# Kernel tuning notes

Hardware: AMD Instinct MI355X
Metric: run time of the kernel (lower is better)

Reference implementation:

```python
import jax, jax.numpy as jnp
import numpy as np

D_MODEL, N_HEADS, N_LEVELS, N_POINTS, ROI = 256, 8, 4, 4, 7
SHAPES = np.array([[100, 150], [50, 75], [25, 38], [13, 19]], dtype=np.int32)
STARTS = np.array([0, 15000, 18750, 19700], dtype=np.int32)


def setup_inputs() -> dict:
    key = jax.random.key(0)
    ks = jax.random.split(key, 12)
    N, Lq = 4, 300
    Len_in = int((SHAPES[:, 0] * SHAPES[:, 1]).sum())  # 19947
    C = D_MODEL
    roi_dim = ROI * ROI * C  # 12544
    np_dim = N_HEADS * N_LEVELS * N_POINTS
    inp = {
        'query': jax.random.normal(ks[0], (N, Lq, C), jnp.float32),
        'reference_points': jax.random.uniform(ks[1], (N, Lq, N_LEVELS, 4), jnp.float32, 0.05, 0.95),
        'input_flatten': jax.random.normal(ks[2], (N, Len_in, C), jnp.float32),
        'input_spatial_shapes': jnp.asarray(SHAPES),
        'input_level_start_index': jnp.asarray(STARTS),
        'input_padding_mask': jnp.zeros((N, Len_in), jnp.bool_),
        'Wv': jax.random.normal(ks[3], (C, C), jnp.float32) / np.sqrt(C),
        'bv': jnp.zeros((C,), jnp.float32),
        'Wp': jax.random.normal(ks[4], (roi_dim, np_dim * 2), jnp.float32) / np.sqrt(roi_dim),
        'bp': jnp.zeros((np_dim * 2,), jnp.float32),
        'Ww': jax.random.normal(ks[5], (roi_dim, np_dim), jnp.float32) / np.sqrt(roi_dim),
        'bw': jnp.zeros((np_dim,), jnp.float32),
        'Wo': jax.random.normal(ks[6], (C, C), jnp.float32) / np.sqrt(C),
        'bo': jnp.zeros((C,), jnp.float32),
    }
    return inp


def _bilinear(img, y, x):
    # img: (H, W, C); y, x: arbitrary shape. Zero padding outside, matches
    # grid_sample(align_corners=False, padding_mode='zeros') / roi_align bilinear.
    H, W = img.shape[0], img.shape[1]
    y0 = jnp.floor(y)
    x0 = jnp.floor(x)
    wy1 = y - y0
    wx1 = x - x0

    def corner(yi, xi, w):
        valid = (yi >= 0) & (yi <= H - 1) & (xi >= 0) & (xi <= W - 1)
        yc = jnp.clip(yi, 0, H - 1).astype(jnp.int32)
        xc = jnp.clip(xi, 0, W - 1).astype(jnp.int32)
        return img[yc, xc] * (w * valid)[..., None]

    return (corner(y0, x0, (1 - wy1) * (1 - wx1))
            + corner(y0, x0 + 1, (1 - wy1) * wx1)
            + corner(y0 + 1, x0, wy1 * (1 - wx1))
            + corner(y0 + 1, x0 + 1, wy1 * wx1))


def _forward(query, reference_points, input_flatten, shapes, starts, padding_mask,
             Wv, bv, Wp, bp, Ww, bw, Wo, bo):
    N, Len_in, C = input_flatten.shape
    Lq = query.shape[1]
    Dh = C // N_HEADS

    # value projection + padding mask
    value = input_flatten @ Wv + bv
    value = jnp.where(padding_mask[..., None], 0.0, value)

    # --- ROI align on level-0 feature map (output 7x7, aligned=True, sampling_ratio=1) ---
    H0, W0 = int(shapes[0, 0]), int(shapes[0, 1])
    v0 = value[:, :H0 * W0].reshape(N, H0, W0, C)
    cx, cy, w, h = [reference_points[:, :, 0, i] for i in range(4)]
    x1 = (cx - 0.5 * w) * W0 - 0.5  # aligned=True offset
    y1 = (cy - 0.5 * h) * H0 - 0.5
    bin_w = (w * W0) / ROI
    bin_h = (h * H0) / ROI
    ctr = jnp.arange(ROI, dtype=jnp.float32) + 0.5  # bin centers
    sx = x1[..., None] + bin_w[..., None] * ctr  # (N, Lq, 7)
    sy = y1[..., None] + bin_h[..., None] * ctr
    yg = jnp.broadcast_to(sy[:, :, :, None], (N, Lq, ROI, ROI))
    xg = jnp.broadcast_to(sx[:, :, None, :], (N, Lq, ROI, ROI))
    roi = jax.vmap(_bilinear)(v0, yg, xg)  # (N, Lq, 7, 7, C)
    roi_flat = roi.reshape(N, Lq, ROI * ROI * C)

    # --- learned sampling points + softmax weights (key_points_sampling_module) ---
    pr = jnp.tanh(roi_flat @ Wp + bp).reshape(N, Lq, N_HEADS, N_LEVELS, N_POINTS, 2)
    logits = (roi_flat @ Ww + bw).reshape(N, Lq, N_HEADS, N_LEVELS * N_POINTS)
    attn = jax.nn.softmax(logits, axis=-1).reshape(N, Lq, N_HEADS, N_LEVELS, N_POINTS)

    # points = ref_center + offsets * ref_wh * 0.5, normalized [0,1], (x, y)
    ref = reference_points  # (N, Lq, L, 4)
    pts = ref[:, :, None, :, None, :2] + pr * ref[:, :, None, :, None, 2:] * 0.5

    # --- multi-scale deformable bilinear sampling ---
    out = jnp.zeros((N, Lq, N_HEADS, Dh), value.dtype)
    value_h = value.reshape(N, Len_in, N_HEADS, Dh)
    for l in range(N_LEVELS):
        Hl, Wl = int(shapes[l, 0]), int(shapes[l, 1])
        s = int(starts[l])
        vl = value_h[:, s:s + Hl * Wl].reshape(N, Hl, Wl, N_HEADS, Dh)
        vl = vl.transpose(0, 3, 1, 2, 4)  # (N, H, Hl, Wl, Dh)
        px = pts[:, :, :, l, :, 0] * Wl - 0.5  # grid_sample align_corners=False
        py = pts[:, :, :, l, :, 1] * Hl - 0.5
        px = px.transpose(0, 2, 1, 3)  # (N, H, Lq, P)
        py = py.transpose(0, 2, 1, 3)
        samp = jax.vmap(jax.vmap(_bilinear))(vl, py, px)  # (N, H, Lq, P, Dh)
        wl = attn[:, :, :, l, :].transpose(0, 2, 1, 3)  # (N, H, Lq, P)
        out = out + jnp.einsum('nhqpd,nhqp->nqhd', samp, wl)

    out = out.reshape(N, Lq, C)
    return out @ Wo + bo


def reference(query, reference_points, input_flatten, input_spatial_shapes,
              input_level_start_index, input_padding_mask,
              Wv, bv, Wp, bp, Ww, bw, Wo, bo):
    shapes = np.asarray(input_spatial_shapes)
    starts = np.asarray(input_level_start_index)
    return _forward(query, reference_points, input_flatten, shapes, starts,
                    input_padding_mask, Wv, bv, Wp, bp, Ww, bw, Wo, bo)
```

## Files before the change

kernel.cpp:

```cpp
#include <hip/hip_runtime.h>
#include <hip/hip_bf16.h>
#include <math.h>

#define NB 4
#define LQ 300
#define CDIM 256
#define NH 8
#define DH 32
#define NL 4
#define NP 4
#define ROI_ 7
#define LEN_IN 19947
#define H0 100
#define W0 150
#define ROI_DIM (ROI_*ROI_*CDIM)
#define NQ_TOT (NB*LQ)
#define QPB 3

#define MPAD2 1280
#define NDIM 384
#define KCH_TOT 196
#define MT_N 10
#define NT_N 3

#define VTOT (NB*LEN_IN)
#define VMT  624

__device__ __constant__ int d_HL[4] = {100, 50, 25, 13};
__device__ __constant__ int d_WL[4] = {150, 75, 38, 19};
__device__ __constant__ int d_ST[4] = {0, 15000, 18750, 19700};

typedef __attribute__((ext_vector_type(8))) short short8;
typedef __attribute__((ext_vector_type(4))) float f32x4;

__device__ __forceinline__ unsigned short f2bf(float f) {
    unsigned int u = __float_as_uint(f);
    unsigned int r = (u + 0x7fffu + ((u >> 16) & 1u)) >> 16;
    return (unsigned short)r;
}
__device__ __forceinline__ float bf2f(unsigned short s) {
    return __uint_as_float(((unsigned int)s) << 16);
}

__device__ __forceinline__ void mfma_32x64(
    const unsigned short* aH, const unsigned short* aL,
    const unsigned short* bH, const unsigned short* bL,
    int wm, int wn, int lr, int kb, f32x4 acc[2][4])
{
    #pragma unroll
    for (int kk = 0; kk < 2; ++kk) {
        short8 ah[2], al[2];
        #pragma unroll
        for (int i = 0; i < 2; ++i) {
            int row = wm * 32 + i * 16 + lr;
            int off = (row * 128 + kk * 64 + kb * 16) ^ ((row & 7) << 4);
            ah[i] = *(const short8*)((const char*)aH + off);
            al[i] = *(const short8*)((const char*)aL + off);
        }
        #pragma unroll
        for (int j = 0; j < 4; ++j) {
            int col = wn * 64 + j * 16 + lr;
            int off = (col * 128 + kk * 64 + kb * 16) ^ ((col & 7) << 4);
            short8 bh = *(const short8*)((const char*)bH + off);
            short8 bl = *(const short8*)((const char*)bL + off);
            #pragma unroll
            for (int i = 0; i < 2; ++i) {
                acc[i][j] = __builtin_amdgcn_mfma_f32_16x16x32_bf16(ah[i], bh, acc[i][j], 0, 0, 0);
                acc[i][j] = __builtin_amdgcn_mfma_f32_16x16x32_bf16(ah[i], bl, acc[i][j], 0, 0, 0);
                acc[i][j] = __builtin_amdgcn_mfma_f32_16x16x32_bf16(al[i], bh, acc[i][j], 0, 0, 0);
            }
        }
    }
}

__global__ __launch_bounds__(256) void k_wvsplit(
    const float* __restrict__ Wv,
    unsigned short* __restrict__ WvTh,
    unsigned short* __restrict__ WvTl)
{
    __shared__ float tile[32][33];
    int k0 = blockIdx.x * 32, c0 = blockIdx.y * 32;
    int tx = threadIdx.x & 31, ty = threadIdx.x >> 5;
    #pragma unroll
    for (int i = 0; i < 4; ++i)
        tile[ty + i * 8][tx] = Wv[(size_t)(k0 + ty + i * 8) * CDIM + c0 + tx];
    __syncthreads();
    #pragma unroll
    for (int i = 0; i < 4; ++i) {
        int c = c0 + ty + i * 8, k = k0 + tx;
        float v = tile[tx][ty + i * 8];
        unsigned short hb = f2bf(v);
        WvTh[(size_t)c * CDIM + k] = hb;
        WvTl[(size_t)c * CDIM + k] = f2bf(v - bf2f(hb));
    }
}

__global__ __launch_bounds__(512, 4) void k_value_mfma(
    const float* __restrict__ inp,
    const unsigned char* __restrict__ mask,
    const unsigned short* __restrict__ WvTh,
    const unsigned short* __restrict__ WvTl,
    const float* __restrict__ bv,
    float* __restrict__ value)
{
    __shared__ unsigned short aH[128 * 64], aL[128 * 64];
    __shared__ unsigned short bH[128 * 64], bL[128 * 64];
    const int row0 = blockIdx.y * 128;
    const int n0 = blockIdx.x * 128;
    const int tid = threadIdx.x;
    const int lane = tid & 63;
    const int wid = tid >> 6;
    const int wm = wid >> 1, wn = wid & 1;
    const int lr = lane & 15, kb = lane >> 4;

    f32x4 acc[2][4];
    #pragma unroll
    for (int i = 0; i < 2; ++i)
        #pragma unroll
        for (int j = 0; j < 4; ++j) acc[i][j] = f32x4{0.f, 0.f, 0.f, 0.f};

    int rc[2], ko[2], growA[2];
    #pragma unroll
    for (int i2 = 0; i2 < 2; ++i2) {
        int slot = tid + i2 * 512;
        rc[i2] = slot >> 3; ko[i2] = slot & 7;
        int g = row0 + rc[i2];
        growA[i2] = (g < VTOT) ? g : (VTOT - 1);
    }

    float4 fa0[2], fa1[2];
    short8 pbh[2], pbl[2];
    #pragma unroll
    for (int i2 = 0; i2 < 2; ++i2) {
        const float* src = inp + (size_t)growA[i2] * CDIM + ko[i2] * 8;
        fa0[i2] = *(const float4*)src;
        fa1[i2] = *(const float4*)(src + 4);
        size_t gb = (size_t)(n0 + rc[i2]) * CDIM + ko[i2] * 8;
        pbh[i2] = *(const short8*)(WvTh + gb);
        pbl[i2] = *(const short8*)(WvTl + gb);
    }

    #pragma unroll
    for (int ch = 0; ch < 4; ++ch) {
        __syncthreads();
        #pragma unroll
        for (int i2 = 0; i2 < 2; ++i2) {
            float f[8] = {fa0[i2].x, fa0[i2].y, fa0[i2].z, fa0[i2].w,
                          fa1[i2].x, fa1[i2].y, fa1[i2].z, fa1[i2].w};
            short8 h, l;
            #pragma unroll
            for (int e = 0; e < 8; ++e) {
                unsigned short hb = f2bf(f[e]);
                h[e] = (short)hb;
                l[e] = (short)f2bf(f[e] - bf2f(hb));
            }
            int off = (rc[i2] * 128 + ko[i2] * 16) ^ ((rc[i2] & 7) << 4);
            *(short8*)((char*)aH + off) = h;
            *(short8*)((char*)aL + off) = l;
            *(short8*)((char*)bH + off) = pbh[i2];
            *(short8*)((char*)bL + off) = pbl[i2];
        }
        __syncthreads();
        if (ch < 3) {
            const int k0n = (ch + 1) * 64;
            #pragma unroll
            for (int i2 = 0; i2 < 2; ++i2) {
                const float* src = inp + (size_t)growA[i2] * CDIM + k0n + ko[i2] * 8;
                fa0[i2] = *(const float4*)src;
                fa1[i2] = *(const float4*)(src + 4);
                size_t gb = (size_t)(n0 + rc[i2]) * CDIM + k0n + ko[i2] * 8;
                pbh[i2] = *(const short8*)(WvTh + gb);
                pbl[i2] = *(const short8*)(WvTl + gb);
            }
        }
        mfma_32x64(aH, aL, bH, bL, wm, wn, lr, kb, acc);
    }

    #pragma unroll
    for (int j = 0; j < 4; ++j) {
        int c = n0 + wn * 64 + j * 16 + lr;
        float b = bv[c];
        #pragma unroll
        for (int i = 0; i < 2; ++i) {
            int q = row0 + wm * 32 + i * 16 + kb * 4;
            #pragma unroll
            for (int e = 0; e < 4; ++e) {
                int row = q + e;
                if (row < VTOT) {
                    float v = acc[i][j][e] + b;
                    if (mask[row]) v = 0.f;
                    value[(size_t)row * CDIM + c] = v;
                }
            }
        }
    }
}

__global__ __launch_bounds__(256) void k_value_proj(
    const float* __restrict__ inp,
    const unsigned char* __restrict__ mask,
    const float* __restrict__ Wv,
    const float* __restrict__ bv,
    float* __restrict__ value)
{
    const int ROWS = 16;
    __shared__ float a_s[ROWS][CDIM];
    const int total = VTOT;
    int row0 = blockIdx.x * ROWS;
    int tid = threadIdx.x;

    #pragma unroll
    for (int r = 0; r < ROWS; ++r) {
        int row = row0 + r;
        a_s[r][tid] = (row < total) ? inp[(size_t)row * CDIM + tid] : 0.f;
    }
    __syncthreads();

    float acc[ROWS];
    #pragma unroll
    for (int r = 0; r < ROWS; ++r) acc[r] = 0.f;

    for (int k = 0; k < CDIM; k += 4) {
        float w0 = Wv[(k + 0) * CDIM + tid];
        float w1 = Wv[(k + 1) * CDIM + tid];
        float w2 = Wv[(k + 2) * CDIM + tid];
        float w3 = Wv[(k + 3) * CDIM + tid];
        #pragma unroll
        for (int r = 0; r < ROWS; ++r) {
            float4 av = *(const float4*)&a_s[r][k];
            acc[r] = fmaf(av.x, w0, fmaf(av.y, w1, fmaf(av.z, w2, fmaf(av.w, w3, acc[r]))));
        }
    }

    float b = bv[tid];
    #pragma unroll
    for (int r = 0; r < ROWS; ++r) {
        int row = row0 + r;
        if (row < total) {
            float v = acc[r] + b;
            if (mask[row]) v = 0.f;
            value[(size_t)row * CDIM + tid] = v;
        }
    }
}

__global__ __launch_bounds__(256) void k_roi_split(
    const float* __restrict__ value,
    const float* __restrict__ refp,
    unsigned short* __restrict__ roiH,
    unsigned short* __restrict__ roiL)
{
    int q = blockIdx.x;
    int t = threadIdx.x;
    int g = t & 31;
    int p8 = t >> 5;

    if (q >= NQ_TOT) {
        short8 z = {0, 0, 0, 0, 0, 0, 0, 0};
        for (int i = p8; i < 49; i += 8) {
            *(short8*)(roiH + (size_t)q * ROI_DIM + i * 256 + g * 8) = z;
            *(short8*)(roiL + (size_t)q * ROI_DIM + i * 256 + g * 8) = z;
        }
        return;
    }
    int n = q / LQ;
    const float* rp = refp + (size_t)q * NL * 4;
    float cx = rp[0], cy = rp[1], w = rp[2], h = rp[3];
    float x1 = (cx - 0.5f * w) * W0 - 0.5f;
    float y1 = (cy - 0.5f * h) * H0 - 0.5f;
    float binw = w * W0 / ROI_;
    float binh = h * H0 / ROI_;
    const float* v0 = value + (size_t)n * LEN_IN * CDIM;

    for (int i = p8; i < 49; i += 8) {
        int r = i / ROI_, c = i % ROI_;
        float sy = y1 + binh * (r + 0.5f);
        float sx = x1 + binw * (c + 0.5f);
        float y0f = floorf(sy), x0f = floorf(sx);
        float wy1 = sy - y0f, wx1 = sx - x0f;
        int y0 = (int)y0f, x0 = (int)x0f;

        float acc[8];
        #pragma unroll
        for (int e = 0; e < 8; ++e) acc[e] = 0.f;

        #pragma unroll
        for (int dy = 0; dy <= 1; ++dy) {
            #pragma unroll
            for (int dx = 0; dx <= 1; ++dx) {
                int yy = y0 + dy, xx = x0 + dx;
                if (yy >= 0 && yy < H0 && xx >= 0 && xx < W0) {
                    float wgt = (dy ? wy1 : 1.f - wy1) * (dx ? wx1 : 1.f - wx1);
                    const float* src = v0 + ((size_t)(yy * W0 + xx)) * CDIM + g * 8;
                    float4 c0 = *(const float4*)src;
                    float4 c1 = *(const float4*)(src + 4);
                    acc[0] += wgt * c0.x; acc[1] += wgt * c0.y;
                    acc[2] += wgt * c0.z; acc[3] += wgt * c0.w;
                    acc[4] += wgt * c1.x; acc[5] += wgt * c1.y;
                    acc[6] += wgt * c1.z; acc[7] += wgt * c1.w;
                }
            }
        }

        short8 hv, lv;
        #pragma unroll
        for (int e = 0; e < 8; ++e) {
            unsigned short hb = f2bf(acc[e]);
            hv[e] = (short)hb;
            lv[e] = (short)f2bf(acc[e] - bf2f(hb));
        }
        *(short8*)(roiH + (size_t)q * ROI_DIM + i * 256 + g * 8) = hv;
        *(short8*)(roiL + (size_t)q * ROI_DIM + i * 256 + g * 8) = lv;
    }
}

__global__ __launch_bounds__(256) void k_wsplit(
    const float* __restrict__ Wp,
    const float* __restrict__ Ww,
    unsigned short* __restrict__ WTh,
    unsigned short* __restrict__ WTl)
{
    __shared__ float tile[32][33];
    int k0 = blockIdx.x * 32, c0 = blockIdx.y * 32;
    int tx = threadIdx.x & 31, ty = threadIdx.x >> 5;

    #pragma unroll
    for (int i = 0; i < 4; ++i) {
        int k = k0 + ty + i * 8, c = c0 + tx;
        float v = (c < 256) ? Wp[(size_t)k * 256 + c] : Ww[(size_t)k * 128 + (c - 256)];
        tile[ty + i * 8][tx] = v;
    }
    __syncthreads();
    #pragma unroll
    for (int i = 0; i < 4; ++i) {
        int c = c0 + ty + i * 8, k = k0 + tx;
        float v = tile[tx][ty + i * 8];
        unsigned short hb = f2bf(v);
        float rem = v - bf2f(hb);
        WTh[(size_t)c * ROI_DIM + k] = hb;
        WTl[(size_t)c * ROI_DIM + k] = f2bf(rem);
    }
}

__global__ __launch_bounds__(512, 4) void k_gemm_bf16x3(
    const unsigned short* __restrict__ roiH,
    const unsigned short* __restrict__ roiL,
    const unsigned short* __restrict__ WTh,
    const unsigned short* __restrict__ WTl,
    float* __restrict__ partials,
    int gch)
{
    __shared__ unsigned short aH[128 * 64], aL[128 * 64];
    __shared__ unsigned short bH[128 * 64], bL[128 * 64];

    const int nwg = gridDim.x;
    const int q8 = nwg >> 3, r8 = nwg & 7;
    const int xcd = blockIdx.x & 7, pos = blockIdx.x >> 3;
    const int start = (xcd < r8) ? xcd * (q8 + 1) : r8 * (q8 + 1) + (xcd - r8) * q8;
    const int lin = start + pos;
    const int mt = lin % MT_N;
    const int t2 = lin / MT_N;
    const int nt = t2 % NT_N;
    const int seg = t2 / NT_N;

    const int q0 = mt * 128, c0 = nt * 128;
    const int tid = threadIdx.x;
    const int lane = tid & 63;
    const int wid = tid >> 6;
    const int wm = wid >> 1, wn = wid & 1;
    const int lr = lane & 15, kb = lane >> 4;

    f32x4 acc[2][4];
    #pragma unroll
    for (int i = 0; i < 2; ++i)
        #pragma unroll
        for (int j = 0; j < 4; ++j) acc[i][j] = f32x4{0.f, 0.f, 0.f, 0.f};

    int rc[2], ko[2];
    #pragma unroll
    for (int i2 = 0; i2 < 2; ++i2) {
        int slot = tid + i2 * 512;
        rc[i2] = slot >> 3; ko[i2] = slot & 7;
    }

    const int kbase = seg * gch * 64;

    short8 pah[2], pal[2], pbh[2], pbl[2];
    #pragma unroll
    for (int i2 = 0; i2 < 2; ++i2) {
        size_t ga = (size_t)(q0 + rc[i2]) * ROI_DIM + kbase + ko[i2] * 8;
        pah[i2] = *(const short8*)(roiH + ga);
        pal[i2] = *(const short8*)(roiL + ga);
        size_t gb = (size_t)(c0 + rc[i2]) * ROI_DIM + kbase + ko[i2] * 8;
        pbh[i2] = *(const short8*)(WTh + gb);
        pbl[i2] = *(const short8*)(WTl + gb);
    }

    for (int ch = 0; ch < gch; ++ch) {
        __syncthreads();
        #pragma unroll
        for (int i2 = 0; i2 < 2; ++i2) {
            int off = (rc[i2] * 128 + ko[i2] * 16) ^ ((rc[i2] & 7) << 4);
            *(short8*)((char*)aH + off) = pah[i2];
            *(short8*)((char*)aL + off) = pal[i2];
            *(short8*)((char*)bH + off) = pbh[i2];
            *(short8*)((char*)bL + off) = pbl[i2];
        }
        __syncthreads();
        if (ch + 1 < gch) {
            const int k0n = kbase + (ch + 1) * 64;
            #pragma unroll
            for (int i2 = 0; i2 < 2; ++i2) {
                size_t ga = (size_t)(q0 + rc[i2]) * ROI_DIM + k0n + ko[i2] * 8;
                pah[i2] = *(const short8*)(roiH + ga);
                pal[i2] = *(const short8*)(roiL + ga);
                size_t gb = (size_t)(c0 + rc[i2]) * ROI_DIM + k0n + ko[i2] * 8;
                pbh[i2] = *(const short8*)(WTh + gb);
                pbl[i2] = *(const short8*)(WTl + gb);
            }
        }
        mfma_32x64(aH, aL, bH, bL, wm, wn, lr, kb, acc);
    }

    #pragma unroll
    for (int i = 0; i < 2; ++i)
        #pragma unroll
        for (int j = 0; j < 4; ++j) {
            int q = q0 + wm * 32 + i * 16 + kb * 4;
            int c = c0 + wn * 64 + j * 16 + lr;
            #pragma unroll
            for (int e = 0; e < 4; ++e)
                partials[((size_t)seg * MPAD2 + q + e) * NDIM + c] = acc[i][j][e];
        }
}

__global__ __launch_bounds__(384) void k_epilogue(
    const float* __restrict__ partials,
    const float* __restrict__ bp, const float* __restrict__ bw,
    float* __restrict__ pr,
    float* __restrict__ attn,
    int nseg)
{
    __shared__ float logit_s[128];
    int q = blockIdx.x;
    int t = threadIdx.x;
    float s = 0.f;
    for (int g = 0; g < nseg; ++g)
        s += partials[((size_t)g * MPAD2 + q) * NDIM + t];
    if (t < 256) {
        pr[(size_t)q * 256 + t] = tanhf(s + bp[t]);
    } else {
        logit_s[t - 256] = s + bw[t - 256];
    }
    __syncthreads();
    if (t < 128) {
        float v = logit_s[t];
        float m = v;
        #pragma unroll
        for (int off = 8; off >= 1; off >>= 1)
            m = fmaxf(m, __shfl_xor(m, off, 16));
        float e = expf(v - m);
        float sum = e;
        #pragma unroll
        for (int off = 8; off >= 1; off >>= 1)
            sum += __shfl_xor(sum, off, 16);
        attn[(size_t)q * 128 + t] = e / sum;
    }
}

__global__ __launch_bounds__(384) void k_roi_gemm(
    const float* __restrict__ value,
    const float* __restrict__ refp,
    const float* __restrict__ Wp,
    const float* __restrict__ bp,
    const float* __restrict__ Ww,
    const float* __restrict__ bw,
    float* __restrict__ pr_out,
    float* __restrict__ attn_out)
{
    __shared__ float roi_s[QPB][ROI_DIM];
    __shared__ float logit_s[QPB][128];

    int tid = threadIdx.x;
    int nq0 = blockIdx.x * QPB;

    for (int qi = 0; qi < QPB; ++qi) {
        int nq = nq0 + qi;
        int n = nq / LQ;
        const float* rp = refp + (size_t)nq * NL * 4;
        float cx = rp[0], cy = rp[1], w = rp[2], h = rp[3];
        float x1 = (cx - 0.5f * w) * W0 - 0.5f;
        float y1 = (cy - 0.5f * h) * H0 - 0.5f;
        float binw = w * W0 / ROI_;
        float binh = h * H0 / ROI_;
        const float* v0 = value + (size_t)n * LEN_IN * CDIM;

        for (int e = tid; e < ROI_DIM; e += 384) {
            int p = e >> 8;
            int ch = e & 255;
            int r = p / ROI_, c = p % ROI_;
            float sy = y1 + binh * (r + 0.5f);
            float sx = x1 + binw * (c + 0.5f);
            float y0f = floorf(sy), x0f = floorf(sx);
            float wy1 = sy - y0f, wx1 = sx - x0f;
            int y0 = (int)y0f, x0 = (int)x0f;
            float acc = 0.f;
            #pragma unroll
            for (int dy = 0; dy <= 1; ++dy)
                #pragma unroll
                for (int dx = 0; dx <= 1; ++dx) {
                    int yy = y0 + dy, xx = x0 + dx;
                    if (yy >= 0 && yy < H0 && xx >= 0 && xx < W0) {
                        float wgt = (dy ? wy1 : 1.f - wy1) * (dx ? wx1 : 1.f - wx1);
                        acc += wgt * v0[((size_t)(yy * W0 + xx)) * CDIM + ch];
                    }
                }
            roi_s[qi][e] = acc;
        }
    }
    __syncthreads();

    int col = tid;
    const float* Wsel;
    int stride;
    float bias;
    if (col < 256) { Wsel = Wp + col;         stride = 256; bias = bp[col]; }
    else           { Wsel = Ww + (col - 256); stride = 128; bias = bw[col - 256]; }

    float acc0 = 0.f, acc1 = 0.f, acc2 = 0.f;
    const float* wptr = Wsel;
    #pragma unroll 8
    for (int k = 0; k < ROI_DIM; ++k) {
        float wv = *wptr; wptr += stride;
        acc0 += roi_s[0][k] * wv;
        acc1 += roi_s[1][k] * wv;
        acc2 += roi_s[2][k] * wv;
    }
    acc0 += bias; acc1 += bias; acc2 += bias;

    if (col < 256) {
        pr_out[(size_t)(nq0 + 0) * 256 + col] = tanhf(acc0);
        pr_out[(size_t)(nq0 + 1) * 256 + col] = tanhf(acc1);
        pr_out[(size_t)(nq0 + 2) * 256 + col] = tanhf(acc2);
    } else {
        int j = col - 256;
        logit_s[0][j] = acc0;
        logit_s[1][j] = acc1;
        logit_s[2][j] = acc2;
    }
    __syncthreads();

    {
        int i = tid & 15;
        int g = tid >> 4;
        int qi = g >> 3, h = g & 7;
        float v = logit_s[qi][h * 16 + i];
        float m = v;
        #pragma unroll
        for (int off = 8; off >= 1; off >>= 1)
            m = fmaxf(m, __shfl_xor(m, off, 16));
        float e = expf(v - m);
        float s = e;
        #pragma unroll
        for (int off = 8; off >= 1; off >>= 1)
            s += __shfl_xor(s, off, 16);
        attn_out[(size_t)(nq0 + qi) * 128 + h * 16 + i] = e / s;
    }
}

__global__ __launch_bounds__(256) void k_sample(
    const float* __restrict__ value,
    const float* __restrict__ refp,
    const float* __restrict__ pr,
    const float* __restrict__ attn,
    float* __restrict__ out_attn)
{
    int nq = blockIdx.x;
    int n = nq / LQ;
    int tid = threadIdx.x;
    int h = tid >> 5, dh = tid & 31;

    float acc = 0.f;
    for (int l = 0; l < NL; ++l) {
        const float* rp = refp + ((size_t)nq * NL + l) * 4;
        float cx = rp[0], cy = rp[1], rw = rp[2], rh = rp[3];
        int Hl = d_HL[l], Wl = d_WL[l], s = d_ST[l];
        const float* vl = value + ((size_t)n * LEN_IN + s) * CDIM;

        #pragma unroll
        for (int p = 0; p < NP; ++p) {
            float prx = pr[(size_t)nq * 256 + h * 32 + l * 8 + p * 2 + 0];
            float pry = pr[(size_t)nq * 256 + h * 32 + l * 8 + p * 2 + 1];
            float a   = attn[(size_t)nq * 128 + h * 16 + l * 4 + p];
            float px = (cx + prx * rw * 0.5f) * Wl - 0.5f;
            float py = (cy + pry * rh * 0.5f) * Hl - 0.5f;
            float x0f = floorf(px), y0f = floorf(py);
            float wx1 = px - x0f, wy1 = py - y0f;
            int x0 = (int)x0f, y0 = (int)y0f;
            float sv = 0.f;
            #pragma unroll
            for (int dy = 0; dy <= 1; ++dy)
                #pragma unroll
                for (int dx = 0; dx <= 1; ++dx) {
                    int yy = y0 + dy, xx = x0 + dx;
                    if (yy >= 0 && yy < Hl && xx >= 0 && xx < Wl) {
                        float wgt = (dy ? wy1 : 1.f - wy1) * (dx ? wx1 : 1.f - wx1);
                        sv += wgt * vl[((size_t)(yy * Wl + xx)) * CDIM + h * 32 + dh];
                    }
                }
            acc += a * sv;
        }
    }
    out_attn[(size_t)nq * CDIM + tid] = acc;
}

__global__ __launch_bounds__(256) void k_out_proj(
    const float* __restrict__ x,
    const float* __restrict__ Wo,
    const float* __restrict__ bo,
    float* __restrict__ out)
{
    const int ROWS = 8;
    __shared__ float a_s[ROWS][CDIM];
    int row0 = blockIdx.x * ROWS;
    int tid = threadIdx.x;

    #pragma unroll
    for (int r = 0; r < ROWS; ++r)
        a_s[r][tid] = x[(size_t)(row0 + r) * CDIM + tid];
    __syncthreads();

    float acc[ROWS];
    #pragma unroll
    for (int r = 0; r < ROWS; ++r) acc[r] = 0.f;

    for (int k = 0; k < CDIM; k += 4) {
        float w0 = Wo[(k + 0) * CDIM + tid];
        float w1 = Wo[(k + 1) * CDIM + tid];
        float w2 = Wo[(k + 2) * CDIM + tid];
        float w3 = Wo[(k + 3) * CDIM + tid];
        #pragma unroll
        for (int r = 0; r < ROWS; ++r) {
            float4 av = *(const float4*)&a_s[r][k];
            acc[r] = fmaf(av.x, w0, fmaf(av.y, w1, fmaf(av.z, w2, fmaf(av.w, w3, acc[r]))));
        }
    }
    float b = bo[tid];
    #pragma unroll
    for (int r = 0; r < ROWS; ++r)
        out[(size_t)(row0 + r) * CDIM + tid] = acc[r] + b;
}

extern "C" void kernel_launch(void* const* d_in, const int* in_sizes, int n_in,
                              void* d_out, int out_size, void* d_ws, size_t ws_size,
                              hipStream_t stream) {
    const float* refp = (const float*)d_in[1];
    const float* inp  = (const float*)d_in[2];
    const unsigned char* mask = (const unsigned char*)d_in[5];
    const float* Wv = (const float*)d_in[6];
    const float* bv = (const float*)d_in[7];
    const float* Wp = (const float*)d_in[8];
    const float* bp = (const float*)d_in[9];
    const float* Ww = (const float*)d_in[10];
    const float* bw = (const float*)d_in[11];
    const float* Wo = (const float*)d_in[12];
    const float* bo = (const float*)d_in[13];
    float* out = (float*)d_out;

    char* ws = (char*)d_ws;
    constexpr size_t VALUE_BYTES = (size_t)VTOT * CDIM * 4;
    constexpr size_t ROI_BYTES   = (size_t)MPAD2 * ROI_DIM * 2;
    constexpr size_t WT_BYTES    = (size_t)NDIM * ROI_DIM * 2;
    constexpr size_t WVT_BYTES   = (size_t)CDIM * CDIM * 2;
    constexpr size_t SEG_BYTES   = (size_t)MPAD2 * NDIM * 4;
    constexpr size_t PR_BYTES    = (size_t)NQ_TOT * 256 * 4;
    constexpr size_t ATTN_BYTES  = (size_t)NQ_TOT * 128 * 4;
    constexpr size_t OA_BYTES    = (size_t)NQ_TOT * 256 * 4;

    size_t off = 0;
    float* value = (float*)(ws + off);                  off += VALUE_BYTES;
    unsigned short* roiH = (unsigned short*)(ws + off); off += ROI_BYTES;
    unsigned short* roiL = (unsigned short*)(ws + off); off += ROI_BYTES;
    unsigned short* WTh  = (unsigned short*)(ws + off); off += WT_BYTES;
    unsigned short* WTl  = (unsigned short*)(ws + off); off += WT_BYTES;
    unsigned short* WvTh = (unsigned short*)(ws + off); off += WVT_BYTES;
    unsigned short* WvTl = (unsigned short*)(ws + off); off += WVT_BYTES;
    const size_t fixed_end = off;
    const size_t tail = PR_BYTES + ATTN_BYTES + OA_BYTES;

    int nseg = 0;
    if (ws_size >= fixed_end + 14 * SEG_BYTES + tail)      nseg = 14;
    else if (ws_size >= fixed_end + 7 * SEG_BYTES + tail)  nseg = 7;

    if (nseg > 0) {
        float* partials = (float*)(ws + fixed_end);
        size_t o2 = fixed_end + (size_t)nseg * SEG_BYTES;
        float* pr       = (float*)(ws + o2); o2 += PR_BYTES;
        float* attn     = (float*)(ws + o2); o2 += ATTN_BYTES;
        float* out_attn = (float*)(ws + o2);

        k_wvsplit<<<dim3(CDIM / 32, CDIM / 32), 256, 0, stream>>>(Wv, WvTh, WvTl);
        k_value_mfma<<<dim3(2, VMT), 512, 0, stream>>>(inp, mask, WvTh, WvTl, bv, value);
        k_roi_split<<<MPAD2, 256, 0, stream>>>(value, refp, roiH, roiL);
        k_wsplit<<<dim3(ROI_DIM / 32, NDIM / 32), 256, 0, stream>>>(Wp, Ww, WTh, WTl);
        k_gemm_bf16x3<<<MT_N * NT_N * nseg, 512, 0, stream>>>(
            roiH, roiL, WTh, WTl, partials, KCH_TOT / nseg);
        k_epilogue<<<NQ_TOT, 384, 0, stream>>>(partials, bp, bw, pr, attn, nseg);
        k_sample<<<NQ_TOT, 256, 0, stream>>>(value, refp, pr, attn, out_attn);
        k_out_proj<<<NQ_TOT / 8, 256, 0, stream>>>(out_attn, Wo, bo, out);
    } else {
        float* pr       = (float*)(ws + VALUE_BYTES);
        float* attn     = (float*)(ws + VALUE_BYTES + PR_BYTES);
        float* out_attn = (float*)(ws + VALUE_BYTES + PR_BYTES + ATTN_BYTES);
        k_value_proj<<<(VTOT + 15) / 16, 256, 0, stream>>>(inp, mask, Wv, bv, value);
        k_roi_gemm<<<NQ_TOT / QPB, 384, 0, stream>>>(value, refp, Wp, bp, Ww, bw, pr, attn);
        k_sample<<<NQ_TOT, 256, 0, stream>>>(value, refp, pr, attn, out_attn);
        k_out_proj<<<NQ_TOT / 8, 256, 0, stream>>>(out_attn, Wo, bo, out);
    }
}
```

Measured before the change: 225.6 us.

## Pre-tile and swizzle GEMM operands, load them with direct global-to-LDS copies

The ROI-split and weight-split kernels now write their bf16 hi/lo operands in a tile-major layout that is already XOR-swizzled to match the LDS layout. The GEMM loads each 64-wide K chunk with global_load_lds 16-byte copies straight into shared memory, so tile data no longer passes through registers. The cost removed is the register staging and the LDS store instructions. In exchange, the old register prefetch of the next chunk is gone, so global loads no longer overlap with the MFMA work, and the two producer kernels now write with scattered, less contiguous stores.

```diff
diff --git a/kernel.cpp b/kernel.cpp
--- a/kernel.cpp
+++ b/kernel.cpp
@@ -40,6 +40,12 @@
 }
 __device__ __forceinline__ float bf2f(unsigned short s) {
     return __uint_as_float(((unsigned int)s) << 16);
+}
+
+__device__ __forceinline__ void gld16(const void* g, void* l) {
+    __builtin_amdgcn_global_load_lds(
+        (const __attribute__((address_space(1))) unsigned int*)g,
+        (__attribute__((address_space(3))) unsigned int*)l, 16, 0, 0);
 }
 
 __device__ __forceinline__ void mfma_32x64(
@@ -247,19 +253,24 @@
 __global__ __launch_bounds__(256) void k_roi_split(
     const float* __restrict__ value,
     const float* __restrict__ refp,
-    unsigned short* __restrict__ roiH,
-    unsigned short* __restrict__ roiL)
+    unsigned short* __restrict__ roiSh,
+    unsigned short* __restrict__ roiSl)
 {
     int q = blockIdx.x;
     int t = threadIdx.x;
     int g = t & 31;
     int p8 = t >> 5;
+    const int mt = q >> 7, r = q & 127;
+    const size_t tbase = (size_t)mt * KCH_TOT * 8192 + (size_t)r * 64;
+    const int swz = ((r & 7) << 3);
 
     if (q >= NQ_TOT) {
         short8 z = {0, 0, 0, 0, 0, 0, 0, 0};
         for (int i = p8; i < 49; i += 8) {
-            *(short8*)(roiH + (size_t)q * ROI_DIM + i * 256 + g * 8) = z;
-            *(short8*)(roiL + (size_t)q * ROI_DIM + i * 256 + g * 8) = z;
+            int k = i * 256 + g * 8;
+            size_t dst = tbase + (size_t)(k >> 6) * 8192 + ((k & 63) ^ swz);
+            *(short8*)(roiSh + dst) = z;
+            *(short8*)(roiSl + dst) = z;
         }
         return;
     }
@@ -273,8 +284,8 @@
     const float* v0 = value + (size_t)n * LEN_IN * CDIM;
 
     for (int i = p8; i < 49; i += 8) {
-        int r = i / ROI_, c = i % ROI_;
-        float sy = y1 + binh * (r + 0.5f);
+        int rr = i / ROI_, c = i % ROI_;
+        float sy = y1 + binh * (rr + 0.5f);
         float sx = x1 + binw * (c + 0.5f);
         float y0f = floorf(sy), x0f = floorf(sx);
         float wy1 = sy - y0f, wx1 = sx - x0f;
@@ -309,16 +320,18 @@
             hv[e] = (short)hb;
             lv[e] = (short)f2bf(acc[e] - bf2f(hb));
         }
-        *(short8*)(roiH + (size_t)q * ROI_DIM + i * 256 + g * 8) = hv;
-        *(short8*)(roiL + (size_t)q * ROI_DIM + i * 256 + g * 8) = lv;
+        int k = i * 256 + g * 8;
+        size_t dst = tbase + (size_t)(k >> 6) * 8192 + ((k & 63) ^ swz);
+        *(short8*)(roiSh + dst) = hv;
+        *(short8*)(roiSl + dst) = lv;
     }
 }
 
 __global__ __launch_bounds__(256) void k_wsplit(
     const float* __restrict__ Wp,
     const float* __restrict__ Ww,
-    unsigned short* __restrict__ WTh,
-    unsigned short* __restrict__ WTl)
+    unsigned short* __restrict__ WTsh,
+    unsigned short* __restrict__ WTsl)
 {
     __shared__ float tile[32][33];
     int k0 = blockIdx.x * 32, c0 = blockIdx.y * 32;
@@ -337,16 +350,19 @@
         float v = tile[tx][ty + i * 8];
         unsigned short hb = f2bf(v);
         float rem = v - bf2f(hb);
-        WTh[(size_t)c * ROI_DIM + k] = hb;
-        WTl[(size_t)c * ROI_DIM + k] = f2bf(rem);
+        int ct = c >> 7, rr = c & 127;
+        size_t dst = ((size_t)(ct * KCH_TOT + (k >> 6)) * 128 + rr) * 64
+                   + ((k & 63) ^ ((rr & 7) << 3));
+        WTsh[dst] = hb;
+        WTsl[dst] = f2bf(rem);
     }
 }
 
 __global__ __launch_bounds__(512, 4) void k_gemm_bf16x3(
-    const unsigned short* __restrict__ roiH,
-    const unsigned short* __restrict__ roiL,
-    const unsigned short* __restrict__ WTh,
-    const unsigned short* __restrict__ WTl,
+    const unsigned short* __restrict__ roiSh,
+    const unsigned short* __restrict__ roiSl,
+    const unsigned short* __restrict__ WTsh,
+    const unsigned short* __restrict__ WTsl,
     float* __restrict__ partials,
     int gch)
 {
@@ -376,49 +392,27 @@
         #pragma unroll
         for (int j = 0; j < 4; ++j) acc[i][j] = f32x4{0.f, 0.f, 0.f, 0.f};
 
-    int rc[2], ko[2];
-    #pragma unroll
-    for (int i2 = 0; i2 < 2; ++i2) {
-        int slot = tid + i2 * 512;
-        rc[i2] = slot >> 3; ko[i2] = slot & 7;
-    }
-
-    const int kbase = seg * gch * 64;
-
-    short8 pah[2], pal[2], pbh[2], pbl[2];
-    #pragma unroll
-    for (int i2 = 0; i2 < 2; ++i2) {
-        size_t ga = (size_t)(q0 + rc[i2]) * ROI_DIM + kbase + ko[i2] * 8;
-        pah[i2] = *(const short8*)(roiH + ga);
-        pal[i2] = *(const short8*)(roiL + ga);
-        size_t gb = (size_t)(c0 + rc[i2]) * ROI_DIM + kbase + ko[i2] * 8;
-        pbh[i2] = *(const short8*)(WTh + gb);
-        pbl[i2] = *(const short8*)(WTl + gb);
-    }
+    const char* Agh = (const char*)roiSh + (size_t)mt * KCH_TOT * 16384;
+    const char* Agl = (const char*)roiSl + (size_t)mt * KCH_TOT * 16384;
+    const char* Bgh = (const char*)WTsh + (size_t)nt * KCH_TOT * 16384;
+    const char* Bgl = (const char*)WTsl + (size_t)nt * KCH_TOT * 16384;
+    const int lb = wid * 2048;
+    const int gl = lb + (lane << 4);
+
+    const int ch0 = seg * gch;
 
     for (int ch = 0; ch < gch; ++ch) {
+        const size_t cb = (size_t)(ch0 + ch) * 16384;
         __syncthreads();
-        #pragma unroll
-        for (int i2 = 0; i2 < 2; ++i2) {
-            int off = (rc[i2] * 128 + ko[i2] * 16) ^ ((rc[i2] & 7) << 4);
-            *(short8*)((char*)aH + off) = pah[i2];
-            *(short8*)((char*)aL + off) = pal[i2];
-            *(short8*)((char*)bH + off) = pbh[i2];
-            *(short8*)((char*)bL + off) = pbl[i2];
-        }
+        gld16(Agh + cb + gl,        (char*)aH + lb);
+        gld16(Agh + cb + gl + 1024, (char*)aH + lb + 1024);
+        gld16(Agl + cb + gl,        (char*)aL + lb);
+        gld16(Agl + cb + gl + 1024, (char*)aL + lb + 1024);
+        gld16(Bgh + cb + gl,        (char*)bH + lb);
+        gld16(Bgh + cb + gl + 1024, (char*)bH + lb + 1024);
+        gld16(Bgl + cb + gl,        (char*)bL + lb);
+        gld16(Bgl + cb + gl + 1024, (char*)bL + lb + 1024);
         __syncthreads();
-        if (ch + 1 < gch) {
-            const int k0n = kbase + (ch + 1) * 64;
-            #pragma unroll
-            for (int i2 = 0; i2 < 2; ++i2) {
-                size_t ga = (size_t)(q0 + rc[i2]) * ROI_DIM + k0n + ko[i2] * 8;
-                pah[i2] = *(const short8*)(roiH + ga);
-                pal[i2] = *(const short8*)(roiL + ga);
-                size_t gb = (size_t)(c0 + rc[i2]) * ROI_DIM + k0n + ko[i2] * 8;
-                pbh[i2] = *(const short8*)(WTh + gb);
-                pbl[i2] = *(const short8*)(WTl + gb);
-            }
-        }
         mfma_32x64(aH, aL, bH, bL, wm, wn, lr, kb, acc);
     }
 
@@ -679,10 +673,10 @@
 
     size_t off = 0;
     float* value = (float*)(ws + off);                  off += VALUE_BYTES;
-    unsigned short* roiH = (unsigned short*)(ws + off); off += ROI_BYTES;
-    unsigned short* roiL = (unsigned short*)(ws + off); off += ROI_BYTES;
-    unsigned short* WTh  = (unsigned short*)(ws + off); off += WT_BYTES;
-    unsigned short* WTl  = (unsigned short*)(ws + off); off += WT_BYTES;
+    unsigned short* roiSh = (unsigned short*)(ws + off); off += ROI_BYTES;
+    unsigned short* roiSl = (unsigned short*)(ws + off); off += ROI_BYTES;
+    unsigned short* WTsh  = (unsigned short*)(ws + off); off += WT_BYTES;
+    unsigned short* WTsl  = (unsigned short*)(ws + off); off += WT_BYTES;
     unsigned short* WvTh = (unsigned short*)(ws + off); off += WVT_BYTES;
     unsigned short* WvTl = (unsigned short*)(ws + off); off += WVT_BYTES;
     const size_t fixed_end = off;
@@ -701,10 +695,10 @@
 
         k_wvsplit<<<dim3(CDIM / 32, CDIM / 32), 256, 0, stream>>>(Wv, WvTh, WvTl);
         k_value_mfma<<<dim3(2, VMT), 512, 0, stream>>>(inp, mask, WvTh, WvTl, bv, value);
-        k_roi_split<<<MPAD2, 256, 0, stream>>>(value, refp, roiH, roiL);
-        k_wsplit<<<dim3(ROI_DIM / 32, NDIM / 32), 256, 0, stream>>>(Wp, Ww, WTh, WTl);
+        k_roi_split<<<MPAD2, 256, 0, stream>>>(value, refp, roiSh, roiSl);
+        k_wsplit<<<dim3(ROI_DIM / 32, NDIM / 32), 256, 0, stream>>>(Wp, Ww, WTsh, WTsl);
         k_gemm_bf16x3<<<MT_N * NT_N * nseg, 512, 0, stream>>>(
-            roiH, roiL, WTh, WTl, partials, KCH_TOT / nseg);
+            roiSh, roiSl, WTsh, WTsl, partials, KCH_TOT / nseg);
         k_epilogue<<<NQ_TOT, 384, 0, stream>>>(partials, bp, bw, pr, attn, nseg);
         k_sample<<<NQ_TOT, 256, 0, stream>>>(value, refp, pr, attn, out_attn);
         k_out_proj<<<NQ_TOT / 8, 256, 0, stream>>>(out_attn, Wo, bo, out);
```

Result: faster. 218.3 us (-3.3%).
